# Kernel tuning notes

Measured on AMD Instinct MI355X. Metric: run time of the kernel, lower is better.

## Reference

```python
import jax, jax.numpy as jnp
import numpy as np

HEADS = 16  # matches init_kwargs


def setup_inputs() -> dict:
    key = jax.random.key(0)
    ks = jax.random.split(key, 9)
    N, L, E, D = 2, 2048, 1024, 64
    return {
        "query": jax.random.normal(ks[0], (N, L, E), dtype=jnp.float32),
        "keys": jax.random.normal(ks[1], (N, L, E), dtype=jnp.float32),
        "values": jax.random.normal(ks[2], (N, L, E), dtype=jnp.float32),
        "masks": jax.random.randint(ks[3], (N, 1, 1, L), 0, 2, dtype=jnp.int32),
        "Wq": jax.random.normal(ks[4], (D, D), dtype=jnp.float32) / np.sqrt(D),
        "Wk": jax.random.normal(ks[5], (D, D), dtype=jnp.float32) / np.sqrt(D),
        "Wv": jax.random.normal(ks[6], (D, D), dtype=jnp.float32) / np.sqrt(D),
        "Wo": jax.random.normal(ks[7], (E, E), dtype=jnp.float32) / np.sqrt(E),
        "bo": jax.random.normal(ks[8], (E,), dtype=jnp.float32),
    }


def reference(query, keys, values, masks, Wq, Wk, Wv, Wo, bo):
    N, Lq, E = query.shape
    Lk = keys.shape[1]
    H = HEADS
    D = E // H
    # split heads: [N, L, H, D]
    q = query.reshape(N, Lq, H, D)
    k = keys.reshape(N, Lk, H, D)
    v = values.reshape(N, Lk, H, D)
    # per-head linear projections (weights shared across heads); Linear: x @ W.T
    q = jnp.einsum("nqhd,ed->nqhe", q, Wq)
    k = jnp.einsum("nkhd,ed->nkhe", k, Wk)
    v = jnp.einsum("nkhd,ed->nkhe", v, Wv)
    # scores [N, H, Lq, Lk]
    scores = jnp.einsum("nqhd,nkhd->nhqk", q, k)
    scores = jnp.where(masks == 0, jnp.float32(-1e20), scores)
    # NOTE: original scales by sqrt(embed_size), not sqrt(head_dim)
    attn = jax.nn.softmax(scores / jnp.sqrt(jnp.float32(E)), axis=3)
    out = jnp.einsum("nhqk,nkhd->nqhd", attn, v).reshape(N, Lq, E)
    return out @ Wo.T + bo
```

## Files before the change

### kernel.cpp

```cpp
#include <hip/hip_runtime.h>


typedef __bf16 bf16_t;
typedef __bf16 bf16x4 __attribute__((ext_vector_type(4)));
typedef __bf16 bf16x8 __attribute__((ext_vector_type(8)));
typedef float f32x4 __attribute__((ext_vector_type(4)));

#define MFMA16(a, b, c) __builtin_amdgcn_mfma_f32_16x16x32_bf16((a), (b), (c), 0, 0, 0)

#define GLOAD_LDS16(gp, lp)                                              \
    __builtin_amdgcn_global_load_lds(                                    \
        (const __attribute__((address_space(1))) void*)(gp),             \
        (__attribute__((address_space(3))) void*)(lp), 16, 0, 0)

__device__ inline bf16x8 cvt8(const float* __restrict__ p, float scale) {
    f32x4 a = *(const f32x4*)p;
    f32x4 b = *(const f32x4*)(p + 4);
    bf16x8 r;
    r[0] = (bf16_t)(a[0] * scale); r[1] = (bf16_t)(a[1] * scale);
    r[2] = (bf16_t)(a[2] * scale); r[3] = (bf16_t)(a[3] * scale);
    r[4] = (bf16_t)(b[0] * scale); r[5] = (bf16_t)(b[1] * scale);
    r[6] = (bf16_t)(b[2] * scale); r[7] = (bf16_t)(b[3] * scale);
    return r;
}

__global__ __launch_bounds__(256) void scan_kernel(const int* __restrict__ msk,
                                                   int* __restrict__ excl)
{
    __shared__ int sums[256];
    const int t = threadIdx.x;
    for (int n = 0; n < 2; n++) {
        const int* m = msk + n * 2048;
        int* e = excl + n * 2049;
        int v[8], s = 0;
        #pragma unroll
        for (int j = 0; j < 8; j++) { v[j] = (m[t * 8 + j] != 0); s += v[j]; }
        sums[t] = s;
        __syncthreads();
        if (t == 0) {
            int a = 0;
            for (int i = 0; i < 256; i++) { int x = sums[i]; sums[i] = a; a += x; }
            e[2048] = a;
        }
        __syncthreads();
        int a = sums[t];
        #pragma unroll
        for (int j = 0; j < 8; j++) { e[t * 8 + j] = a; a += v[j]; }
        __syncthreads();
    }
}

__global__ __launch_bounds__(256) void qkv_proj_kernel(
    const float* __restrict__ qin, const float* __restrict__ kin,
    const float* __restrict__ vin,
    const float* __restrict__ Wq, const float* __restrict__ Wk,
    const float* __restrict__ Wv, const float* __restrict__ Wo,
    const int* __restrict__ excl,
    bf16_t* __restrict__ qp, bf16_t* __restrict__ kc, bf16_t* __restrict__ vcT,
    bf16_t* __restrict__ Wob)
{
    __shared__ bf16_t Ct[64][72];
    __shared__ short mapS[64];

    const int t = threadIdx.x;
    const int w = t >> 6, lane = t & 63, quad = lane >> 4, l16 = lane & 15;

    if (blockIdx.y == 3) {
        int idx = blockIdx.x * 1024 + t * 4;
        f32x4 v = *(const f32x4*)&Wo[idx];
        bf16x4 r;
        r[0] = (bf16_t)v[0]; r[1] = (bf16_t)v[1];
        r[2] = (bf16_t)v[2]; r[3] = (bf16_t)v[3];
        *(bf16x4*)&Wob[idx] = r;
        return;
    }

    if (blockIdx.y == 2) {
        const int h = blockIdx.x & 15;
        const int tb = (blockIdx.x >> 4) * 64;
        const int n = tb >> 11, l0 = tb & 2047;
        const int tg = tb + w * 16 + l16;

        bf16x8 b0 = cvt8(&vin[(size_t)tg * 1024 + h * 64 + quad * 8], 1.0f);
        bf16x8 b1 = cvt8(&vin[(size_t)tg * 1024 + h * 64 + 32 + quad * 8], 1.0f);

        const int cbase = excl[n * 2049 + l0];
        const int cnt   = excl[n * 2049 + l0 + 64] - cbase;
        if (t < 64) {
            int c  = excl[n * 2049 + l0 + t];
            int c1 = excl[n * 2049 + l0 + t + 1];
            if (c1 > c) mapS[c - cbase] = (short)t;
        }

        #pragma unroll
        for (int nt = 0; nt < 4; nt++) {
            bf16x8 a0 = cvt8(&Wv[(nt * 16 + l16) * 64 + quad * 8], 1.0f);
            bf16x8 a1 = cvt8(&Wv[(nt * 16 + l16) * 64 + 32 + quad * 8], 1.0f);
            f32x4 acc = {0.f, 0.f, 0.f, 0.f};
            acc = MFMA16(a0, b0, acc);
            acc = MFMA16(a1, b1, acc);
            #pragma unroll
            for (int r = 0; r < 4; r++)
                Ct[nt * 16 + quad * 4 + r][w * 16 + l16] = (bf16_t)acc[r];
        }
        __syncthreads();
        const int p = t & 63, rg = t >> 6;
        if (p < cnt) {
            int j = mapS[p];
            size_t ob = ((size_t)(n * 16 + h)) * 131072 + cbase + p;
            #pragma unroll
            for (int rr = 0; rr < 16; rr++) {
                int r = rg * 16 + rr;
                vcT[ob + (size_t)r * 2048] = Ct[r][j];
            }
        }
        return;
    }

    const bool isK = (blockIdx.y == 1);
    const float* x; const float* W; bf16_t* outp; float scale;
    if (!isK) { x = qin; W = Wq; outp = qp; scale = 0.03125f; }
    else      { x = kin; W = Wk; outp = kc; scale = 1.0f; }

    const int g0 = blockIdx.x * 64;
    bf16x8 a0 = cvt8(&x[(size_t)(g0 + w * 16 + l16) * 64 + quad * 8], scale);
    bf16x8 a1 = cvt8(&x[(size_t)(g0 + w * 16 + l16) * 64 + 32 + quad * 8], scale);

    #pragma unroll
    for (int nt = 0; nt < 4; nt++) {
        bf16x8 b0 = cvt8(&W[(nt * 16 + l16) * 64 + quad * 8], 1.0f);
        bf16x8 b1 = cvt8(&W[(nt * 16 + l16) * 64 + 32 + quad * 8], 1.0f);
        f32x4 acc = {0.f, 0.f, 0.f, 0.f};
        acc = MFMA16(a0, b0, acc);
        acc = MFMA16(a1, b1, acc);
        #pragma unroll
        for (int r = 0; r < 4; r++)
            Ct[w * 16 + quad * 4 + r][nt * 16 + l16] = (bf16_t)acc[r];
    }
    __syncthreads();
    #pragma unroll
    for (int it = 0; it < 2; it++) {
        int j = it * 32 + (t >> 3);
        int g = g0 + j, h2 = g & 15, token = g >> 4;
        int n2 = token >> 11, l = token & 2047;
        if (isK) {
            int c  = excl[n2 * 2049 + l];
            int c1 = excl[n2 * 2049 + l + 1];
            if (c1 > c)
                *(bf16x8*)&outp[(((size_t)(n2 * 16 + h2)) * 2048 + c) * 64 + (t & 7) * 8] =
                    *(const bf16x8*)&Ct[j][(t & 7) * 8];
        } else {
            *(bf16x8*)&outp[(((size_t)(n2 * 16 + h2)) * 2048 + l) * 64 + (t & 7) * 8] =
                *(const bf16x8*)&Ct[j][(t & 7) * 8];
        }
    }
}

__global__ __launch_bounds__(256) void attn_kernel(
    const bf16_t* __restrict__ qp, const bf16_t* __restrict__ kc,
    const bf16_t* __restrict__ vcT, const int* __restrict__ excl,
    bf16_t* __restrict__ ao)
{
    __shared__ bf16_t Kt[2][64][64];
    __shared__ bf16_t Vt[2][64][64];
    __shared__ bf16_t PwT[4][32][72];

    const int t = threadIdx.x;
    const int w = t >> 6, lane = t & 63, quad = lane >> 4, l16 = lane & 15;

    const int flat = blockIdx.x;
    const int xcd = flat & 7, slot = flat >> 3;
    const int nh = xcd * 4 + (slot >> 4), qb = slot & 15;
    const int n = nh >> 4, h = nh & 15;
    const int qbase = qb * 128 + w * 32;
    const size_t nhbase = (size_t)nh * 131072;

    const int Lc = excl[n * 2049 + 2048];
    const int ntiles = (Lc + 63) >> 6;

    bf16x8 aq[2][2];
    #pragma unroll
    for (int qs = 0; qs < 2; qs++)
        #pragma unroll
        for (int c = 0; c < 2; c++)
            aq[qs][c] = *(const bf16x8*)&qp[nhbase + (size_t)(qbase + qs * 16 + l16) * 64 + c * 32 + quad * 8];

    f32x4 o[2][4];
    float lsum[2] = {0.f, 0.f};
    #pragma unroll
    for (int qs = 0; qs < 2; qs++)
        #pragma unroll
        for (int dt = 0; dt < 4; dt++) {
            o[qs][dt][0] = 0.f; o[qs][dt][1] = 0.f; o[qs][dt][2] = 0.f; o[qs][dt][3] = 0.f;
        }

    const int kwbase = w * 16;

    #pragma unroll
    for (int j = 0; j < 2; j++) {
        int rb = kwbase + j * 8;
        GLOAD_LDS16(&kc[nhbase + (size_t)rb * 64 + lane * 8], &Kt[0][rb][0]);
        GLOAD_LDS16(&vcT[nhbase + (size_t)(rb + (lane >> 3)) * 2048 + (lane & 7) * 8],
                    &Vt[0][rb][0]);
    }

    for (int i = 0; i < ntiles; i++) {
        const int cb = i & 1, nb = cb ^ 1;
        const int k0 = i * 64;
        __syncthreads();

        if (i + 1 < ntiles) {
            const int kn = k0 + 64;
            #pragma unroll
            for (int j = 0; j < 2; j++) {
                int rb = kwbase + j * 8;
                GLOAD_LDS16(&kc[nhbase + (size_t)(kn + rb) * 64 + lane * 8], &Kt[nb][rb][0]);
                GLOAD_LDS16(&vcT[nhbase + (size_t)(rb + (lane >> 3)) * 2048 + kn + (lane & 7) * 8],
                            &Vt[nb][rb][0]);
            }
        }

        f32x4 st[2][4];
        #pragma unroll
        for (int ct = 0; ct < 4; ct++) {
            bf16x8 kb0 = *(const bf16x8*)&Kt[cb][ct * 16 + l16][quad * 8];
            bf16x8 kb1 = *(const bf16x8*)&Kt[cb][ct * 16 + l16][32 + quad * 8];
            #pragma unroll
            for (int qs = 0; qs < 2; qs++) {
                f32x4 acc = {0.f, 0.f, 0.f, 0.f};
                acc = MFMA16(kb0, aq[qs][0], acc);
                acc = MFMA16(kb1, aq[qs][1], acc);
                st[qs][ct] = acc;
            }
        }

        if (k0 + 64 <= Lc) {
            #pragma unroll
            for (int ct = 0; ct < 4; ct++)
                #pragma unroll
                for (int qs = 0; qs < 2; qs++) {
                    bf16x4 pk;
                    #pragma unroll
                    for (int r = 0; r < 4; r++) {
                        float p = __expf(st[qs][ct][r]);
                        lsum[qs] += p;
                        pk[r] = (bf16_t)p;
                    }
                    *(bf16x4*)&PwT[w][qs * 16 + l16][ct * 16 + quad * 4] = pk;
                }
        } else {
            #pragma unroll
            for (int ct = 0; ct < 4; ct++)
                #pragma unroll
                for (int qs = 0; qs < 2; qs++) {
                    bf16x4 pk;
                    #pragma unroll
                    for (int r = 0; r < 4; r++) {
                        int kk = k0 + ct * 16 + quad * 4 + r;
                        float p = (kk < Lc) ? __expf(st[qs][ct][r]) : 0.0f;
                        lsum[qs] += p;
                        pk[r] = (bf16_t)p;
                    }
                    *(bf16x4*)&PwT[w][qs * 16 + l16][ct * 16 + quad * 4] = pk;
                }
        }
        asm volatile("s_waitcnt lgkmcnt(0)" ::: "memory");

        bf16x8 bp[2][2];
        #pragma unroll
        for (int qs = 0; qs < 2; qs++) {
            bp[qs][0] = *(const bf16x8*)&PwT[w][qs * 16 + l16][quad * 8];
            bp[qs][1] = *(const bf16x8*)&PwT[w][qs * 16 + l16][32 + quad * 8];
        }
        #pragma unroll
        for (int dt = 0; dt < 4; dt++) {
            bf16x8 va0 = *(const bf16x8*)&Vt[cb][dt * 16 + l16][quad * 8];
            bf16x8 va1 = *(const bf16x8*)&Vt[cb][dt * 16 + l16][32 + quad * 8];
            #pragma unroll
            for (int qs = 0; qs < 2; qs++) {
                o[qs][dt] = MFMA16(va0, bp[qs][0], o[qs][dt]);
                o[qs][dt] = MFMA16(va1, bp[qs][1], o[qs][dt]);
            }
        }
    }

    #pragma unroll
    for (int qs = 0; qs < 2; qs++) {
        float v = lsum[qs];
        v += __shfl_xor(v, 16);
        v += __shfl_xor(v, 32);
        float inv = 1.0f / v;
        const int q = qbase + qs * 16 + l16;
        const size_t base = ((size_t)n * 2048 + q) * 1024 + h * 64;
        #pragma unroll
        for (int dt = 0; dt < 4; dt++) {
            bf16x4 ov;
            #pragma unroll
            for (int r = 0; r < 4; r++) ov[r] = (bf16_t)(o[qs][dt][r] * inv);
            *(bf16x4*)&ao[base + dt * 16 + quad * 4] = ov;
        }
    }
}

__global__ __launch_bounds__(256, 2) void out_proj_kernel(
    const bf16_t* __restrict__ X, const bf16_t* __restrict__ Wob,
    const float* __restrict__ bo, float* __restrict__ out)
{
    __shared__ bf16_t Xs[2][128][64];
    __shared__ bf16_t Ws[2][64][64];

    const int t = threadIdx.x;
    const int w = t >> 6, lane = t & 63, quad = lane >> 4, l16 = lane & 15;
    const int Mbase = blockIdx.x * 128;
    const int Nbase = blockIdx.y * 64;
    const int mrow = (w & 1) * 64;
    const int ncol = (w >> 1) * 32;

    f32x4 acc[4][2];
    #pragma unroll
    for (int mi = 0; mi < 4; mi++)
        #pragma unroll
        for (int ni = 0; ni < 2; ni++) {
            acc[mi][ni][0] = 0.f; acc[mi][ni][1] = 0.f;
            acc[mi][ni][2] = 0.f; acc[mi][ni][3] = 0.f;
        }

    #pragma unroll
    for (int j = 0; j < 4; j++) {
        int br = w * 32 + j * 8;
        GLOAD_LDS16(&X[(size_t)(Mbase + br + (lane >> 3)) * 1024 + (lane & 7) * 8],
                    &Xs[0][br][0]);
    }
    #pragma unroll
    for (int j = 0; j < 2; j++) {
        int br = w * 16 + j * 8;
        GLOAD_LDS16(&Wob[(size_t)(Nbase + br + (lane >> 3)) * 1024 + (lane & 7) * 8],
                    &Ws[0][br][0]);
    }

    for (int i = 0; i < 16; i++) {
        const int cb = i & 1, nb = cb ^ 1;
        __syncthreads();

        if (i < 15) {
            const int kn = (i + 1) * 64;
            #pragma unroll
            for (int j = 0; j < 4; j++) {
                int br = w * 32 + j * 8;
                GLOAD_LDS16(&X[(size_t)(Mbase + br + (lane >> 3)) * 1024 + kn + (lane & 7) * 8],
                            &Xs[nb][br][0]);
            }
            #pragma unroll
            for (int j = 0; j < 2; j++) {
                int br = w * 16 + j * 8;
                GLOAD_LDS16(&Wob[(size_t)(Nbase + br + (lane >> 3)) * 1024 + kn + (lane & 7) * 8],
                            &Ws[nb][br][0]);
            }
        }

        #pragma unroll
        for (int c = 0; c < 2; c++) {
            bf16x8 bfr[2];
            #pragma unroll
            for (int ni = 0; ni < 2; ni++)
                bfr[ni] = *(const bf16x8*)&Ws[cb][ncol + ni * 16 + l16][c * 32 + quad * 8];
            #pragma unroll
            for (int mi = 0; mi < 4; mi++) {
                bf16x8 afr = *(const bf16x8*)&Xs[cb][mrow + mi * 16 + l16][c * 32 + quad * 8];
                #pragma unroll
                for (int ni = 0; ni < 2; ni++)
                    acc[mi][ni] = MFMA16(afr, bfr[ni], acc[mi][ni]);
            }
        }
    }

    #pragma unroll
    for (int ni = 0; ni < 2; ni++) {
        float b = bo[Nbase + ncol + ni * 16 + l16];
        #pragma unroll
        for (int mi = 0; mi < 4; mi++) {
            #pragma unroll
            for (int r = 0; r < 4; r++) {
                int row = Mbase + mrow + mi * 16 + quad * 4 + r;
                out[(size_t)row * 1024 + Nbase + ncol + ni * 16 + l16] = acc[mi][ni][r] + b;
            }
        }
    }
}

extern "C" void kernel_launch(void* const* d_in, const int* in_sizes, int n_in,
                              void* d_out, int out_size, void* d_ws, size_t ws_size,
                              hipStream_t stream)
{
    const float* qin = (const float*)d_in[0];
    const float* kin = (const float*)d_in[1];
    const float* vin = (const float*)d_in[2];
    const int*   msk = (const int*)d_in[3];
    const float* Wq  = (const float*)d_in[4];
    const float* Wk  = (const float*)d_in[5];
    const float* Wv  = (const float*)d_in[6];
    const float* Wo  = (const float*)d_in[7];
    const float* bo  = (const float*)d_in[8];
    float* out = (float*)d_out;

    bf16_t* ws  = (bf16_t*)d_ws;
    bf16_t* qp  = ws;
    bf16_t* kc  = ws + 4194304;
    bf16_t* vcT = ws + 8388608;
    bf16_t* ao  = ws + 12582912;
    bf16_t* Wob = ws + 16777216;
    int* excl   = (int*)(ws + 17825792);

    scan_kernel<<<1, 256, 0, stream>>>(msk, excl);
    qkv_proj_kernel<<<dim3(1024, 4), 256, 0, stream>>>(qin, kin, vin, Wq, Wk, Wv, Wo,
                                                        excl, qp, kc, vcT, Wob);
    attn_kernel<<<dim3(512), 256, 0, stream>>>(qp, kc, vcT, excl, ao);
    out_proj_kernel<<<dim3(32, 16), 256, 0, stream>>>(ao, Wob, bo, out);
}
```

Measured before the change: 186.9 us.

## Process 128 rows per block in Q/K projection with LDS-staged input loads

The Q/K projection path now handles 128 rows per block instead of 64, and blocks with index 512 or higher exit early. Input rows are staged into shared memory with direct global-to-LDS loads, then converted. Each W fragment is reused across two row subtiles. Shared memory grows to a 51 KB union buffer, which may reduce occupancy and leaves half the launched Q/K blocks idle.

```diff
diff --git a/kernel.cpp b/kernel.cpp
--- a/kernel.cpp
+++ b/kernel.cpp
@@ -59,8 +59,7 @@
     bf16_t* __restrict__ qp, bf16_t* __restrict__ kc, bf16_t* __restrict__ vcT,
     bf16_t* __restrict__ Wob)
 {
-    __shared__ bf16_t Ct[64][72];
-    __shared__ short mapS[64];
+    __shared__ __align__(16) char smem[51200];
 
     const int t = threadIdx.x;
     const int w = t >> 6, lane = t & 63, quad = lane >> 4, l16 = lane & 15;
@@ -76,6 +75,8 @@
     }
 
     if (blockIdx.y == 2) {
+        bf16_t* Ct = (bf16_t*)smem;
+        short* mapS = (short*)(smem + 16384);
         const int h = blockIdx.x & 15;
         const int tb = (blockIdx.x >> 4) * 64;
         const int n = tb >> 11, l0 = tb & 2047;
@@ -101,7 +102,7 @@
             acc = MFMA16(a1, b1, acc);
             #pragma unroll
             for (int r = 0; r < 4; r++)
-                Ct[nt * 16 + quad * 4 + r][w * 16 + l16] = (bf16_t)acc[r];
+                Ct[(nt * 16 + quad * 4 + r) * 72 + w * 16 + l16] = (bf16_t)acc[r];
         }
         __syncthreads();
         const int p = t & 63, rg = t >> 6;
@@ -111,47 +112,74 @@
             #pragma unroll
             for (int rr = 0; rr < 16; rr++) {
                 int r = rg * 16 + rr;
-                vcT[ob + (size_t)r * 2048] = Ct[r][j];
+                vcT[ob + (size_t)r * 2048] = Ct[r * 72 + j];
             }
         }
         return;
     }
 
+    if (blockIdx.x >= 512) return;
     const bool isK = (blockIdx.y == 1);
-    const float* x; const float* W; bf16_t* outp; float scale;
-    if (!isK) { x = qin; W = Wq; outp = qp; scale = 0.03125f; }
-    else      { x = kin; W = Wk; outp = kc; scale = 1.0f; }
-
-    const int g0 = blockIdx.x * 64;
-    bf16x8 a0 = cvt8(&x[(size_t)(g0 + w * 16 + l16) * 64 + quad * 8], scale);
-    bf16x8 a1 = cvt8(&x[(size_t)(g0 + w * 16 + l16) * 64 + 32 + quad * 8], scale);
-
+    const float* x; const float* W; float scale;
+    if (!isK) { x = qin; W = Wq; scale = 0.03125f; }
+    else      { x = kin; W = Wk; scale = 1.0f; }
+
+    float* Xs = (float*)smem;
+    bf16_t* Ct2 = (bf16_t*)(smem + 32768);
+
+    const int g0 = blockIdx.x * 128;
+
+    #pragma unroll
+    for (int j = 0; j < 8; j++) {
+        int br = w * 32 + j * 4;
+        GLOAD_LDS16(&x[(size_t)(g0 + br) * 64 + lane * 4], &Xs[br * 64]);
+    }
+    __syncthreads();
+
+    const int rbase = w * 32;
+    bf16x8 a[2][2];
+    #pragma unroll
+    for (int qs = 0; qs < 2; qs++)
+        #pragma unroll
+        for (int c = 0; c < 2; c++)
+            a[qs][c] = cvt8(&Xs[(rbase + qs * 16 + l16) * 64 + c * 32 + quad * 8], scale);
+
+    f32x4 acc[4][2];
     #pragma unroll
     for (int nt = 0; nt < 4; nt++) {
         bf16x8 b0 = cvt8(&W[(nt * 16 + l16) * 64 + quad * 8], 1.0f);
         bf16x8 b1 = cvt8(&W[(nt * 16 + l16) * 64 + 32 + quad * 8], 1.0f);
-        f32x4 acc = {0.f, 0.f, 0.f, 0.f};
-        acc = MFMA16(a0, b0, acc);
-        acc = MFMA16(a1, b1, acc);
-        #pragma unroll
-        for (int r = 0; r < 4; r++)
-            Ct[w * 16 + quad * 4 + r][nt * 16 + l16] = (bf16_t)acc[r];
-    }
+        #pragma unroll
+        for (int qs = 0; qs < 2; qs++) {
+            f32x4 z = {0.f, 0.f, 0.f, 0.f};
+            z = MFMA16(a[qs][0], b0, z);
+            z = MFMA16(a[qs][1], b1, z);
+            acc[nt][qs] = z;
+        }
+    }
+
+    #pragma unroll
+    for (int nt = 0; nt < 4; nt++)
+        #pragma unroll
+        for (int qs = 0; qs < 2; qs++)
+            #pragma unroll
+            for (int r = 0; r < 4; r++)
+                Ct2[(rbase + qs * 16 + quad * 4 + r) * 72 + nt * 16 + l16] = (bf16_t)acc[nt][qs][r];
     __syncthreads();
-    #pragma unroll
-    for (int it = 0; it < 2; it++) {
+
+    #pragma unroll
+    for (int it = 0; it < 4; it++) {
         int j = it * 32 + (t >> 3);
         int g = g0 + j, h2 = g & 15, token = g >> 4;
         int n2 = token >> 11, l = token & 2047;
+        bf16x8 val = *(const bf16x8*)&Ct2[j * 72 + (t & 7) * 8];
         if (isK) {
             int c  = excl[n2 * 2049 + l];
             int c1 = excl[n2 * 2049 + l + 1];
             if (c1 > c)
-                *(bf16x8*)&outp[(((size_t)(n2 * 16 + h2)) * 2048 + c) * 64 + (t & 7) * 8] =
-                    *(const bf16x8*)&Ct[j][(t & 7) * 8];
+                *(bf16x8*)&kc[(((size_t)(n2 * 16 + h2)) * 2048 + c) * 64 + (t & 7) * 8] = val;
         } else {
-            *(bf16x8*)&outp[(((size_t)(n2 * 16 + h2)) * 2048 + l) * 64 + (t & 7) * 8] =
-                *(const bf16x8*)&Ct[j][(t & 7) * 8];
+            *(bf16x8*)&qp[(((size_t)(n2 * 16 + h2)) * 2048 + l) * 64 + (t & 7) * 8] = val;
         }
     }
 }
```

After: 185.2 us. Within noise of the previous version (-0.9%).
